# Performance work log

Measured on AMD Instinct MI355X. Metric: run time of the kernel, lower is better.

## Reference

```python
import jax, jax.numpy as jnp
import numpy as np

B, T, C = 32, 1024, 512
D = C // 2          # reduction_factor_input = 2 -> conv1d(1x1) filters = 256
U = 256             # LSTM units
O = U // 1          # reduction_factor_output = 1 -> 256


def setup_inputs() -> dict:
    key = jax.random.key(0)
    ks = jax.random.split(key, 8)
    s = lambda *d: 1.0 / np.sqrt(d[0])
    return {
        "x": jax.random.normal(ks[0], (B, T, C), jnp.float32),
        "w_in": jax.random.normal(ks[1], (C, D), jnp.float32) * s(C),
        "b_in": jnp.zeros((D,), jnp.float32),
        "kernel": jax.random.normal(ks[2], (D, 4 * U), jnp.float32) * s(D),
        "rec_kernel": jax.random.normal(ks[3], (U, 4 * U), jnp.float32) * s(U),
        "bias": jnp.zeros((4 * U,), jnp.float32),
        "w_out": jax.random.normal(ks[4], (U, O), jnp.float32) * s(U),
        "b_out": jnp.zeros((O,), jnp.float32),
    }


def _lstm(xz, rec_kernel):
    # xz: [T, B, 4U] precomputed input projection (x @ kernel + bias)
    def step(carry, xt):
        h, c = carry
        z = xt + h @ rec_kernel  # [B, 4U]
        i, f, g, o = jnp.split(z, 4, axis=-1)  # Keras gate order: i, f, c, o
        i = jax.nn.sigmoid(i)
        f = jax.nn.sigmoid(f)
        g = jnp.tanh(g)
        o = jax.nn.sigmoid(o)
        c = f * c + i * g
        h = o * jnp.tanh(c)
        return (h, c), h

    b = xz.shape[1]
    init = (jnp.zeros((b, U), xz.dtype), jnp.zeros((b, U), xz.dtype))
    _, hs = jax.lax.scan(step, init, xz)
    return hs  # [T, B, U]


def reference(x, w_in, b_in, kernel, rec_kernel, bias, w_out, b_out):
    # Conv1D kernel_size=1 == per-timestep dense projection
    xin = x @ w_in + b_in                      # [B, T, D]
    xz = xin @ kernel + bias                   # [B, T, 4U]
    hs = _lstm(jnp.transpose(xz, (1, 0, 2)), rec_kernel)  # [T, B, U]
    hs = jnp.transpose(hs, (1, 0, 2))          # [B, T, U]
    return hs @ w_out + b_out                  # [B, T, O]
```

## Files before the change

### kernel.cpp

```cpp
#include <hip/hip_runtime.h>


#define DEV static __device__ __forceinline__

typedef __attribute__((ext_vector_type(8))) short short8;
typedef __attribute__((ext_vector_type(4))) float floatx4;
typedef _Float16 half8 __attribute__((ext_vector_type(8)));

static constexpr int Bsz = 32, T = 1024, C = 512, D = 256, U = 256, FU = 1024;
static constexpr int M = Bsz * T;

DEV float bfu2f(unsigned int u) { union { unsigned int i; float f; } v; v.i = u; return v.f; }
DEV float bf2f(unsigned short u) { return bfu2f(((unsigned int)u) << 16); }
DEV unsigned short f2bf(float f) {
    union { float f; unsigned int i; } v; v.f = f;
    return (unsigned short)((v.i + 0x7fffu + ((v.i >> 16) & 1u)) >> 16);
}
DEV float sigmf(float x) { return 1.0f / (1.0f + __expf(-x)); }
DEV float tanhfast(float x) {
    const float a = __expf(-2.0f * fabsf(x));
    const float t = (1.0f - a) / (1.0f + a);
    return copysignf(t, x);
}
DEV half8 h8c(uint4 v) { return __builtin_bit_cast(half8, v); }

DEV short ld_bf(const float* p) { return (short)f2bf(*p); }
DEV short ld_bf(const unsigned short* p) { return (short)*p; }
DEV short8 ld_frag(const unsigned short* p) { return *(const short8*)p; }
DEV short8 ld_frag(const float* p) {
    short8 v;
#pragma unroll
    for (int j = 0; j < 8; j++) v[j] = (short)f2bf(p[j]);
    return v;
}
DEV float ldxz1(const float* p) { return *p; }
DEV float ldxz1(const unsigned short* p) { return bf2f(*p); }

#define BAR() asm volatile("s_waitcnt lgkmcnt(0)\n\ts_barrier" ::: "memory")

template <int K, int N, int MT, int NS, bool OUTF32, typename AT, typename BT>
__global__ __launch_bounds__(64) void gemm_mfma(
    const AT* __restrict__ A,
    const BT* __restrict__ Bm,
    const float* __restrict__ bias,
    void* __restrict__ Cv)
{
    constexpr int KC = K / 32;
    const int lane = threadIdx.x;
    const int quad = lane >> 4, lr = lane & 15;
    constexpr int NSG = N / (16 * NS);
    const int sg = blockIdx.x % NSG;
    const int mb = blockIdx.x / NSG;
    const int n0 = sg * 16 * NS;

    short8 bf[NS][KC];
    float biasv[NS];
#pragma unroll
    for (int s = 0; s < NS; s++) {
        const int n = n0 + s * 16 + lr;
        biasv[s] = bias[n];
#pragma unroll
        for (int kc = 0; kc < KC; kc++) {
            short8 v;
#pragma unroll
            for (int j = 0; j < 8; j++) {
                const int k = kc * 32 + quad * 8 + j;
                v[j] = ld_bf(&Bm[(size_t)k * N + n]);
            }
            bf[s][kc] = v;
        }
    }

    for (int mt = 0; mt < MT; mt++) {
        const int m0 = (mb * MT + mt) * 16;
        const AT* Ap = A + (size_t)(m0 + lr) * K + quad * 8;
        floatx4 acc[NS];
#pragma unroll
        for (int s = 0; s < NS; s++) acc[s] = (floatx4){0.f, 0.f, 0.f, 0.f};
#pragma unroll
        for (int kc = 0; kc < KC; kc++) {
            short8 af = ld_frag(Ap + kc * 32);
#pragma unroll
            for (int s = 0; s < NS; s++)
                acc[s] = __builtin_amdgcn_mfma_f32_16x16x32_bf16(af, bf[s][kc], acc[s], 0, 0, 0);
        }
#pragma unroll
        for (int s = 0; s < NS; s++) {
            const int n = n0 + s * 16 + lr;
#pragma unroll
            for (int r = 0; r < 4; r++) {
                const int m = m0 + quad * 4 + r;
                const float val = acc[s][r] + biasv[s];
                if (OUTF32)
                    ((float*)Cv)[(size_t)m * N + n] = val;
                else
                    ((unsigned short*)Cv)[(size_t)m * N + n] = f2bf(val);
            }
        }
    }
}

__global__ __launch_bounds__(256) void pack_rec_mfma(const float* __restrict__ rec,
                                                     uint4* __restrict__ Pm)
{
    const int idx = blockIdx.x * 256 + threadIdx.x;
    const int lane = idx & 63;
    const int kc = (idx >> 6) & 7;
    const int strip = idx >> 9;
    const int q = lane >> 4, lr = lane & 15;
    const int col = strip * 16 + lr;
    const int k0 = kc * 32 + q * 8;
    union { unsigned short u[8]; uint4 v; } out;
#pragma unroll
    for (int j = 0; j < 8; j++) {
        const _Float16 h = (_Float16)rec[(size_t)(k0 + j) * FU + col];
        out.u[j] = __builtin_bit_cast(unsigned short, h);
    }
    Pm[idx] = out.v;
}

template <typename XZT>
__global__ __launch_bounds__(512, 2)
void lstm_bcast(
    const XZT* __restrict__ xz,
    const uint4* __restrict__ Pm,
    unsigned short* __restrict__ hs)
{
    const int b = blockIdx.x;
    const int tid = threadIdx.x;
    const int w = tid >> 6;
    const int lane = tid & 63;
    const int q = lane >> 4, lr = lane & 15;

    __shared__ uint4 Wl[16 * 8 * 64];
    __shared__ __align__(16) unsigned short h_pk[2][U];

    for (int i = tid; i < 16 * 8 * 64; i += 512) {
        const int sl = i >> 9;
        const int gs = 48 + 2 * (sl >> 1) + (sl & 1);
        Wl[i] = Pm[(size_t)gs * 512 + (i & 511)];
    }
    if (tid < 128) { ((unsigned int*)h_pk[0])[tid] = 0; }

    uint4 Wa0[8], Wa1[8], Wa2[8], Wa3[8];
    uint4 Wv0[8], Wv1[8];
#pragma unroll
    for (int kc = 0; kc < 8; kc++) {
        Wa0[kc] = Pm[((size_t)(2 * w + 0) * 8 + kc) * 64 + lane];
        Wa1[kc] = Pm[((size_t)(2 * w + 1) * 8 + kc) * 64 + lane];
        Wa2[kc] = Pm[((size_t)(16 + 2 * w) * 8 + kc) * 64 + lane];
        Wa3[kc] = Pm[((size_t)(17 + 2 * w) * 8 + kc) * 64 + lane];
        Wv0[kc] = Pm[((size_t)(32 + 2 * w) * 8 + kc) * 64 + lane];
        Wv1[kc] = Pm[((size_t)(33 + 2 * w) * 8 + kc) * 64 + lane];
    }
#pragma unroll
    for (int kc = 0; kc < 8; kc++) {
        asm volatile("" : "+a"(Wa0[kc].x), "+a"(Wa0[kc].y), "+a"(Wa0[kc].z), "+a"(Wa0[kc].w));
        asm volatile("" : "+a"(Wa1[kc].x), "+a"(Wa1[kc].y), "+a"(Wa1[kc].z), "+a"(Wa1[kc].w));
        asm volatile("" : "+a"(Wa2[kc].x), "+a"(Wa2[kc].y), "+a"(Wa2[kc].z), "+a"(Wa2[kc].w));
        asm volatile("" : "+a"(Wa3[kc].x), "+a"(Wa3[kc].y), "+a"(Wa3[kc].z), "+a"(Wa3[kc].w));
        asm volatile("" : "+v"(Wv0[kc].x), "+v"(Wv0[kc].y), "+v"(Wv0[kc].z), "+v"(Wv0[kc].w));
        asm volatile("" : "+v"(Wv1[kc].x), "+v"(Wv1[kc].y), "+v"(Wv1[kc].z), "+v"(Wv1[kc].w));
    }
    __syncthreads();

    const XZT* xzb = xz + (size_t)b * T * FU;
    unsigned short* hsb = hs + (size_t)b * T * U;

    const int u = 32 * w + 16 * q + lr;
    const bool gact = (q < 2);

    float cst = 0.f;
    float xzi = 0.f, xzf = 0.f, xzg = 0.f, xzo = 0.f;
    if (gact) {
        xzi = ldxz1(xzb + u);        xzf = ldxz1(xzb + 256 + u);
        xzg = ldxz1(xzb + 512 + u);  xzo = ldxz1(xzb + 768 + u);
    }

    for (int t = 0; t < T; t++) {
        float xzi_n = 0.f, xzf_n = 0.f, xzg_n = 0.f, xzo_n = 0.f;
        if (gact && t + 1 < T) {
            const XZT* xt = xzb + (size_t)(t + 1) * FU;
            xzi_n = ldxz1(xt + u);       xzf_n = ldxz1(xt + 256 + u);
            xzg_n = ldxz1(xt + 512 + u); xzo_n = ldxz1(xt + 768 + u);
        }

        const char* hb = ((const char*)h_pk) + (t & 1) * 512;

        floatx4 a0 = {0.f,0.f,0.f,0.f}, a1 = {0.f,0.f,0.f,0.f};
        floatx4 a2 = {0.f,0.f,0.f,0.f}, a3 = {0.f,0.f,0.f,0.f};
        floatx4 a4 = {0.f,0.f,0.f,0.f}, a5 = {0.f,0.f,0.f,0.f};
        floatx4 a6 = {0.f,0.f,0.f,0.f}, a7 = {0.f,0.f,0.f,0.f};

        uint4 afc = *(const uint4*)(hb + q * 16), afn;
#pragma unroll
        for (int kc = 0; kc < 8; kc++) {
            if (kc < 7) afn = *(const uint4*)(hb + (kc + 1) * 64 + q * 16);
            const uint4 s6 = Wl[((w * 2 + 0) * 8 + kc) * 64 + lane];
            const uint4 s7 = Wl[((w * 2 + 1) * 8 + kc) * 64 + lane];
            const half8 av = h8c(afc);
            a0 = __builtin_amdgcn_mfma_f32_16x16x32_f16(av, h8c(Wa0[kc]), a0, 0, 0, 0);
            a1 = __builtin_amdgcn_mfma_f32_16x16x32_f16(av, h8c(Wa1[kc]), a1, 0, 0, 0);
            a2 = __builtin_amdgcn_mfma_f32_16x16x32_f16(av, h8c(Wa2[kc]), a2, 0, 0, 0);
            a3 = __builtin_amdgcn_mfma_f32_16x16x32_f16(av, h8c(Wa3[kc]), a3, 0, 0, 0);
            a4 = __builtin_amdgcn_mfma_f32_16x16x32_f16(av, h8c(Wv0[kc]), a4, 0, 0, 0);
            a5 = __builtin_amdgcn_mfma_f32_16x16x32_f16(av, h8c(Wv1[kc]), a5, 0, 0, 0);
            a6 = __builtin_amdgcn_mfma_f32_16x16x32_f16(av, h8c(s6), a6, 0, 0, 0);
            a7 = __builtin_amdgcn_mfma_f32_16x16x32_f16(av, h8c(s7), a7, 0, 0, 0);
            afc = afn;
        }

        if (gact) {
            float zi_, zf_, zg_, zo_;
            if (q == 0) { zi_ = a0[0]; zf_ = a2[0]; zg_ = a4[0]; zo_ = a6[0]; }
            else        { zi_ = a1[0]; zf_ = a3[0]; zg_ = a5[0]; zo_ = a7[0]; }
            const float iv = sigmf(zi_ + xzi);
            const float fv = sigmf(zf_ + xzf);
            const float gv = tanhfast(zg_ + xzg);
            const float ov = sigmf(zo_ + xzo);
            cst = fv * cst + iv * gv;
            const float hv = ov * tanhfast(cst);
            h_pk[(t + 1) & 1][u] = __builtin_bit_cast(unsigned short, (_Float16)hv);
            hsb[(size_t)t * U + u] = f2bf(hv);
        }
        BAR();

        xzi = xzi_n; xzf = xzf_n; xzg = xzg_n; xzo = xzo_n;
    }
}

extern "C" void kernel_launch(void* const* d_in, const int* in_sizes, int n_in,
                              void* d_out, int out_size, void* d_ws, size_t ws_size,
                              hipStream_t stream)
{
    const float* x    = (const float*)d_in[0];
    const float* w_in = (const float*)d_in[1];
    const float* b_in = (const float*)d_in[2];
    const float* kern = (const float*)d_in[3];
    const float* rec  = (const float*)d_in[4];
    const float* bias = (const float*)d_in[5];
    const float* wout = (const float*)d_in[6];
    const float* bout = (const float*)d_in[7];

    char* ws = (char*)d_ws;
    const size_t rec_bytes = (size_t)64 * 8 * 64 * 16;
    const size_t xin_bytes = (size_t)M * D * 2;
    const size_t hs_bytes  = (size_t)M * U * 2;
    const size_t xz32_bytes = (size_t)M * FU * 4;
    const size_t base = rec_bytes + xin_bytes + hs_bytes;

    uint4* Pm = (uint4*)ws;
    unsigned short* xin_bf = (unsigned short*)(ws + rec_bytes);
    unsigned short* hs_bf  = (unsigned short*)(ws + rec_bytes + xin_bytes);
    char* xz_raw = ws + base;

    const bool use_f32 = ws_size >= base + xz32_bytes;

    pack_rec_mfma<<<128, 256, 0, stream>>>(rec, Pm);

    gemm_mfma<512, 256, 16, 2, false><<<(256 / 32) * (M / 256), 64, 0, stream>>>(
        x, w_in, b_in, (void*)xin_bf);

    if (use_f32) {
        float* xzp = (float*)xz_raw;
        gemm_mfma<256, 1024, 16, 2, true><<<(1024 / 32) * (M / 256), 64, 0, stream>>>(
            xin_bf, kern, bias, (void*)xzp);
        lstm_bcast<float><<<Bsz, 512, 0, stream>>>(xzp, Pm, hs_bf);
    } else {
        unsigned short* xzp = (unsigned short*)xz_raw;
        gemm_mfma<256, 1024, 16, 2, false><<<(1024 / 32) * (M / 256), 64, 0, stream>>>(
            xin_bf, kern, bias, (void*)xzp);
        lstm_bcast<unsigned short><<<Bsz, 512, 0, stream>>>(xzp, Pm, hs_bf);
    }

    gemm_mfma<256, 256, 16, 2, true><<<(256 / 32) * (M / 256), 64, 0, stream>>>(
        hs_bf, wout, bout, d_out);
}
```

Before: 1.881 ms.

## Replace per-step block barrier with per-wave LDS flags in LSTM recurrence

The per-timestep workgroup barrier in the LSTM kernel is replaced by per-wave progress flags in shared memory. Each wave spins only on the flag of the wave that produced the hidden-state chunk it needs next. The k-chunk order is rotated per wave so each wave starts with the chunk it wrote itself, which lets waves start the next step before the slowest wave finishes. This relies on correct LDS ordering across the double-buffered h, and busy-wait polling adds LDS traffic and the risk of spinning.

```diff
diff --git a/kernel.cpp b/kernel.cpp
--- a/kernel.cpp
+++ b/kernel.cpp
@@ -36,7 +36,7 @@
 DEV float ldxz1(const float* p) { return *p; }
 DEV float ldxz1(const unsigned short* p) { return bf2f(*p); }
 
-#define BAR() asm volatile("s_waitcnt lgkmcnt(0)\n\ts_barrier" ::: "memory")
+#define LGKM0() asm volatile("s_waitcnt lgkmcnt(0)" ::: "memory")
 
 template <int K, int N, int MT, int NS, bool OUTF32, typename AT, typename BT>
 __global__ __launch_bounds__(64) void gemm_mfma(
@@ -121,7 +121,7 @@
 
 template <typename XZT>
 __global__ __launch_bounds__(512, 2)
-void lstm_bcast(
+void lstm_flow(
     const XZT* __restrict__ xz,
     const uint4* __restrict__ Pm,
     unsigned short* __restrict__ hs)
@@ -134,6 +134,7 @@
 
     __shared__ uint4 Wl[16 * 8 * 64];
     __shared__ __align__(16) unsigned short h_pk[2][U];
+    __shared__ volatile unsigned int flags[8];
 
     for (int i = tid; i < 16 * 8 * 64; i += 512) {
         const int sl = i >> 9;
@@ -141,26 +142,28 @@
         Wl[i] = Pm[(size_t)gs * 512 + (i & 511)];
     }
     if (tid < 128) { ((unsigned int*)h_pk[0])[tid] = 0; }
+    if (tid < 8) flags[tid] = 0u;
 
     uint4 Wa0[8], Wa1[8], Wa2[8], Wa3[8];
     uint4 Wv0[8], Wv1[8];
 #pragma unroll
-    for (int kc = 0; kc < 8; kc++) {
-        Wa0[kc] = Pm[((size_t)(2 * w + 0) * 8 + kc) * 64 + lane];
-        Wa1[kc] = Pm[((size_t)(2 * w + 1) * 8 + kc) * 64 + lane];
-        Wa2[kc] = Pm[((size_t)(16 + 2 * w) * 8 + kc) * 64 + lane];
-        Wa3[kc] = Pm[((size_t)(17 + 2 * w) * 8 + kc) * 64 + lane];
-        Wv0[kc] = Pm[((size_t)(32 + 2 * w) * 8 + kc) * 64 + lane];
-        Wv1[kc] = Pm[((size_t)(33 + 2 * w) * 8 + kc) * 64 + lane];
-    }
-#pragma unroll
-    for (int kc = 0; kc < 8; kc++) {
-        asm volatile("" : "+a"(Wa0[kc].x), "+a"(Wa0[kc].y), "+a"(Wa0[kc].z), "+a"(Wa0[kc].w));
-        asm volatile("" : "+a"(Wa1[kc].x), "+a"(Wa1[kc].y), "+a"(Wa1[kc].z), "+a"(Wa1[kc].w));
-        asm volatile("" : "+a"(Wa2[kc].x), "+a"(Wa2[kc].y), "+a"(Wa2[kc].z), "+a"(Wa2[kc].w));
-        asm volatile("" : "+a"(Wa3[kc].x), "+a"(Wa3[kc].y), "+a"(Wa3[kc].z), "+a"(Wa3[kc].w));
-        asm volatile("" : "+v"(Wv0[kc].x), "+v"(Wv0[kc].y), "+v"(Wv0[kc].z), "+v"(Wv0[kc].w));
-        asm volatile("" : "+v"(Wv1[kc].x), "+v"(Wv1[kc].y), "+v"(Wv1[kc].z), "+v"(Wv1[kc].w));
+    for (int j = 0; j < 8; j++) {
+        const int kc = (w + j) & 7;
+        Wa0[j] = Pm[((size_t)(2 * w + 0) * 8 + kc) * 64 + lane];
+        Wa1[j] = Pm[((size_t)(2 * w + 1) * 8 + kc) * 64 + lane];
+        Wa2[j] = Pm[((size_t)(16 + 2 * w) * 8 + kc) * 64 + lane];
+        Wa3[j] = Pm[((size_t)(17 + 2 * w) * 8 + kc) * 64 + lane];
+        Wv0[j] = Pm[((size_t)(32 + 2 * w) * 8 + kc) * 64 + lane];
+        Wv1[j] = Pm[((size_t)(33 + 2 * w) * 8 + kc) * 64 + lane];
+    }
+#pragma unroll
+    for (int j = 0; j < 8; j++) {
+        asm volatile("" : "+a"(Wa0[j].x), "+a"(Wa0[j].y), "+a"(Wa0[j].z), "+a"(Wa0[j].w));
+        asm volatile("" : "+a"(Wa1[j].x), "+a"(Wa1[j].y), "+a"(Wa1[j].z), "+a"(Wa1[j].w));
+        asm volatile("" : "+a"(Wa2[j].x), "+a"(Wa2[j].y), "+a"(Wa2[j].z), "+a"(Wa2[j].w));
+        asm volatile("" : "+a"(Wa3[j].x), "+a"(Wa3[j].y), "+a"(Wa3[j].z), "+a"(Wa3[j].w));
+        asm volatile("" : "+v"(Wv0[j].x), "+v"(Wv0[j].y), "+v"(Wv0[j].z), "+v"(Wv0[j].w));
+        asm volatile("" : "+v"(Wv1[j].x), "+v"(Wv1[j].y), "+v"(Wv1[j].z), "+v"(Wv1[j].w));
     }
     __syncthreads();
 
@@ -192,19 +195,26 @@
         floatx4 a4 = {0.f,0.f,0.f,0.f}, a5 = {0.f,0.f,0.f,0.f};
         floatx4 a6 = {0.f,0.f,0.f,0.f}, a7 = {0.f,0.f,0.f,0.f};
 
-        uint4 afc = *(const uint4*)(hb + q * 16), afn;
-#pragma unroll
-        for (int kc = 0; kc < 8; kc++) {
-            if (kc < 7) afn = *(const uint4*)(hb + (kc + 1) * 64 + q * 16);
+        uint4 afc = *(const uint4*)(hb + w * 64 + q * 16), afn;
+
+#pragma unroll
+        for (int j = 0; j < 8; j++) {
+            const int kc = (w + j) & 7;
+            if (j < 7) {
+                const int kcn = (w + j + 1) & 7;
+                while (flags[kcn] < (unsigned int)t) { }
+                LGKM0();
+                afn = *(const uint4*)(hb + kcn * 64 + q * 16);
+            }
             const uint4 s6 = Wl[((w * 2 + 0) * 8 + kc) * 64 + lane];
             const uint4 s7 = Wl[((w * 2 + 1) * 8 + kc) * 64 + lane];
             const half8 av = h8c(afc);
-            a0 = __builtin_amdgcn_mfma_f32_16x16x32_f16(av, h8c(Wa0[kc]), a0, 0, 0, 0);
-            a1 = __builtin_amdgcn_mfma_f32_16x16x32_f16(av, h8c(Wa1[kc]), a1, 0, 0, 0);
-            a2 = __builtin_amdgcn_mfma_f32_16x16x32_f16(av, h8c(Wa2[kc]), a2, 0, 0, 0);
-            a3 = __builtin_amdgcn_mfma_f32_16x16x32_f16(av, h8c(Wa3[kc]), a3, 0, 0, 0);
-            a4 = __builtin_amdgcn_mfma_f32_16x16x32_f16(av, h8c(Wv0[kc]), a4, 0, 0, 0);
-            a5 = __builtin_amdgcn_mfma_f32_16x16x32_f16(av, h8c(Wv1[kc]), a5, 0, 0, 0);
+            a0 = __builtin_amdgcn_mfma_f32_16x16x32_f16(av, h8c(Wa0[j]), a0, 0, 0, 0);
+            a1 = __builtin_amdgcn_mfma_f32_16x16x32_f16(av, h8c(Wa1[j]), a1, 0, 0, 0);
+            a2 = __builtin_amdgcn_mfma_f32_16x16x32_f16(av, h8c(Wa2[j]), a2, 0, 0, 0);
+            a3 = __builtin_amdgcn_mfma_f32_16x16x32_f16(av, h8c(Wa3[j]), a3, 0, 0, 0);
+            a4 = __builtin_amdgcn_mfma_f32_16x16x32_f16(av, h8c(Wv0[j]), a4, 0, 0, 0);
+            a5 = __builtin_amdgcn_mfma_f32_16x16x32_f16(av, h8c(Wv1[j]), a5, 0, 0, 0);
             a6 = __builtin_amdgcn_mfma_f32_16x16x32_f16(av, h8c(s6), a6, 0, 0, 0);
             a7 = __builtin_amdgcn_mfma_f32_16x16x32_f16(av, h8c(s7), a7, 0, 0, 0);
             afc = afn;
@@ -223,7 +233,8 @@
             h_pk[(t + 1) & 1][u] = __builtin_bit_cast(unsigned short, (_Float16)hv);
             hsb[(size_t)t * U + u] = f2bf(hv);
         }
-        BAR();
+        LGKM0();
+        if (lane == 0) flags[w] = (unsigned int)(t + 1);
 
         xzi = xzi_n; xzf = xzf_n; xzg = xzg_n; xzo = xzo_n;
     }
@@ -265,12 +276,12 @@
         float* xzp = (float*)xz_raw;
         gemm_mfma<256, 1024, 16, 2, true><<<(1024 / 32) * (M / 256), 64, 0, stream>>>(
             xin_bf, kern, bias, (void*)xzp);
-        lstm_bcast<float><<<Bsz, 512, 0, stream>>>(xzp, Pm, hs_bf);
+        lstm_flow<float><<<Bsz, 512, 0, stream>>>(xzp, Pm, hs_bf);
     } else {
         unsigned short* xzp = (unsigned short*)xz_raw;
         gemm_mfma<256, 1024, 16, 2, false><<<(1024 / 32) * (M / 256), 64, 0, stream>>>(
             xin_bf, kern, bias, (void*)xzp);
-        lstm_bcast<unsigned short><<<Bsz, 512, 0, stream>>>(xzp, Pm, hs_bf);
+        lstm_flow<unsigned short><<<Bsz, 512, 0, stream>>>(xzp, Pm, hs_bf);
     }
 
     gemm_mfma<256, 256, 16, 2, true><<<(256 / 32) * (M / 256), 64, 0, stream>>>(
```

After: 4.312 ms. +129.2%, slower.
